# Kernel optimization log

Measured on AMD Instinct MI355X. Metric: run time of the kernel, lower is better.

The kernel has to match this reference:

```python
import jax, jax.numpy as jnp
import numpy as np

NUM_CLASSES = 4
SIGMA_S = 1.0
SIGMA_Z = 1.0


def _rbf_gram(x, sigma):
    # x: [N, d] -> [N, N] Gaussian kernel exp(-||xi-xj||^2 / (2 sigma^2))
    sq = jnp.sum(x * x, axis=-1)
    d2 = sq[:, None] + sq[None, :] - 2.0 * (x @ x.T)
    d2 = jnp.maximum(d2, 0.0)
    return jnp.exp(-d2 / (2.0 * sigma * sigma))


def _double_center(K):
    # Faithful to: K = mean_center(K, dim=0); K_m = mean_center(K.t(), dim=0)
    K = K - jnp.mean(K, axis=0, keepdims=True)
    K = K.T
    K = K - jnp.mean(K, axis=0, keepdims=True)
    return K


def setup_inputs() -> dict:
    key = jax.random.key(0)
    kz, ks = jax.random.split(key)
    z = jax.random.normal(kz, (8192, 128), dtype=jnp.float32)
    s = jax.random.randint(ks, (8192,), 0, NUM_CLASSES, dtype=jnp.int64)
    norm = jnp.float32(1.0)
    return {"z": z, "s": s, "norm": norm}


def reference(z, s, norm):
    n = z.shape[0]
    s_onehot = jax.nn.one_hot(s, NUM_CLASSES, dtype=z.dtype)  # format_onehot
    K_sm = _double_center(_rbf_gram(s_onehot, SIGMA_S))
    K_zm = _double_center(_rbf_gram(z, SIGMA_Z))
    # trace(K_zm.T @ K_sm) == sum(K_zm * K_sm): O(N^2) instead of O(N^3)
    dep = jnp.sum(K_zm * K_sm)
    dep = dep / (norm * (n * n))
    return dep
```

## Files before the change

kernel.cpp:

```cpp
#include <hip/hip_runtime.h>
#include <hip/hip_bf16.h>

typedef float f32x4 __attribute__((ext_vector_type(4)));

#define ZD      128
#define BT      128
#define D2_CUT  60.0f
#define D2_TRIG 70.0f

__device__ __forceinline__ void async_copy16(const unsigned char* g,
                                             unsigned char* l) {
    __builtin_amdgcn_global_load_lds(
        (const __attribute__((address_space(1))) unsigned int*)g,
        (__attribute__((address_space(3))) unsigned int*)l,
        16, 0, 0);
}

__global__ __launch_bounds__(256) void dep_prep(
    const float* __restrict__ z, const int* __restrict__ s,
    float* __restrict__ sq, float* __restrict__ sqmin,
    unsigned char* __restrict__ zb8, float* __restrict__ pvals,
    const float* __restrict__ norm, float* __restrict__ out, int N)
{
    __shared__ float part[32][33];
    const int tid  = threadIdx.x;
    const int wave = tid >> 6, lane = tid & 63;
    const int half = lane >> 5, c = lane & 31;
    const int r0   = blockIdx.x * 32;

    if (blockIdx.x == 0 && wave == 2) {
        int c0 = 0, c1 = 0, c2 = 0, c3 = 0;
        for (int it = lane; it < N / 4; it += 64) {
            int4 v = ((const int4*)s)[it];
            c0 += (v.x == 0) + (v.y == 0) + (v.z == 0) + (v.w == 0);
            c1 += (v.x == 1) + (v.y == 1) + (v.z == 1) + (v.w == 1);
            c2 += (v.x == 2) + (v.y == 2) + (v.z == 2) + (v.w == 2);
            c3 += (v.x == 3) + (v.y == 3) + (v.z == 3) + (v.w == 3);
        }
        #pragma unroll
        for (int off = 1; off < 64; off <<= 1) {
            c0 += __shfl_xor(c0, off, 64);
            c1 += __shfl_xor(c1, off, 64);
            c2 += __shfl_xor(c2, off, 64);
            c3 += __shfl_xor(c3, off, 64);
        }
        if (lane == 0) {
            const double n = (double)N;
            const double p0 = c0 / n, p1 = c1 / n, p2 = c2 / n, p3 = c3 / n;
            const double sump2 = p0*p0 + p1*p1 + p2*p2 + p3*p3;
            const double scale = (1.0 - exp(-1.0)) / ((double)norm[0] * n * n);
            pvals[0] = (float)p0; pvals[1] = (float)p1;
            pvals[2] = (float)p2; pvals[3] = (float)p3;
            pvals[4] = (float)sump2;
            pvals[5] = (float)scale;
            const double c2sum = (double)c0*c0 + (double)c1*c1
                               + (double)c2*c2 + (double)c3*c3;
            const double diag = n - c2sum / n;
            out[0] = (float)(diag * scale);
        }
    }

    #pragma unroll
    for (int i = 0; i < 4; ++i) {
        const int rloc = wave * 8 + i * 2 + half;
        const int r    = r0 + rloc;
        float4 v = ((const float4*)z)[r * 32 + c];
        int pk = __builtin_amdgcn_cvt_pk_fp8_f32(v.x, v.y, 0, false);
        pk     = __builtin_amdgcn_cvt_pk_fp8_f32(v.z, v.w, pk, true);
        ((unsigned int*)zb8)[r * 32 + c] = (unsigned int)pk;
        part[rloc][c] = v.x*v.x + v.y*v.y + v.z*v.z + v.w*v.w;
    }
    __syncthreads();

    if (wave == 0 && lane < 32) {
        float sum = 0.f;
        #pragma unroll
        for (int k = 0; k < 32; ++k) sum += part[lane][k];
        sq[r0 + lane] = sum;
        float mn = sum;
        #pragma unroll
        for (int off = 1; off < 32; off <<= 1)
            mn = fminf(mn, __shfl_xor(mn, off, 64));
        if (lane == 0) sqmin[blockIdx.x] = mn;
    }
}

__global__ __launch_bounds__(256, 4) void dep_pair(
    const unsigned char* __restrict__ zb8, const float* __restrict__ sq,
    const float* __restrict__ sqmin, const int* __restrict__ s,
    const float* __restrict__ pvals, float* __restrict__ out, int T)
{
    __shared__ unsigned char Apan[BT * ZD];
    __shared__ unsigned char Bpan[BT * ZD];

    const int tid  = threadIdx.x;
    const int wave = tid >> 6, lane = tid & 63;

    const int t = blockIdx.x;
    #define TRI_BASE(x) ((x) * T - ((x) * ((x) - 1)) / 2)
    double disc = (2.0 * T + 1.0) * (2.0 * T + 1.0) - 8.0 * (double)t;
    int ti = (int)((2.0 * T + 1.0 - sqrt(disc)) * 0.5);
    if (ti < 0) ti = 0;
    if (ti > T - 1) ti = T - 1;
    while (ti + 1 < T && TRI_BASE(ti + 1) <= t) ++ti;
    while (ti > 0 && TRI_BASE(ti) > t) --ti;
    const int tj = ti + (t - TRI_BASE(ti));
    #undef TRI_BASE

    const int i0 = ti * BT, j0 = tj * BT;
    const int wi = wave >> 1, wj = wave & 1;
    const int l15 = lane & 15, quad = lane >> 4;

    {
        const unsigned char* gAp = zb8 + (size_t)i0 * ZD;
        const unsigned char* gBp = zb8 + (size_t)j0 * ZD;
        const int rl  = lane >> 3;
        const int cch = lane & 7;
        const int gch = cch ^ rl;
        #pragma unroll
        for (int k = 0; k < 4; ++k) {
            const int r0i = (wave * 4 + k) * 8;
            const size_t go = (size_t)(r0i + rl) * ZD + (gch << 4);
            async_copy16(gAp + go, Apan + r0i * ZD);
            async_copy16(gBp + go, Bpan + r0i * ZD);
        }
    }
    __syncthreads();

    f32x4 accv[4][4];
    #pragma unroll
    for (int a = 0; a < 4; ++a)
        #pragma unroll
        for (int b = 0; b < 4; ++b)
            accv[a][b] = (f32x4){0.f, 0.f, 0.f, 0.f};

    const int sub = (quad & 1) * 8;
    #pragma unroll
    for (int kc = 0; kc < 4; ++kc) {
        long af[4], bfr[4];
        const int ch = (kc * 2 + (quad >> 1)) ^ (l15 & 7);
        #pragma unroll
        for (int it = 0; it < 4; ++it) {
            const int row = wi * 64 + it * 16 + l15;
            af[it] = *(const long*)(Apan + row * ZD + (ch << 4) + sub);
        }
        #pragma unroll
        for (int jt = 0; jt < 4; ++jt) {
            const int row = wj * 64 + jt * 16 + l15;
            bfr[jt] = *(const long*)(Bpan + row * ZD + (ch << 4) + sub);
        }
        #pragma unroll
        for (int it = 0; it < 4; ++it)
            #pragma unroll
            for (int jt = 0; jt < 4; ++jt)
                accv[it][jt] = __builtin_amdgcn_mfma_f32_16x16x32_fp8_fp8(
                    af[it], bfr[jt], accv[it][jt], 0, 0, 0);
    }

    float m = -1e30f;
    #pragma unroll
    for (int it = 0; it < 4; ++it)
        #pragma unroll
        for (int jt = 0; jt < 4; ++jt) {
            const f32x4 v = accv[it][jt];
            m = fmaxf(m, fmaxf(fmaxf(v[0], v[1]), fmaxf(v[2], v[3])));
        }
    #pragma unroll
    for (int off = 1; off < 64; off <<= 1)
        m = fmaxf(m, __shfl_xor(m, off, 64));

    const int gA = (i0 >> 5) + wi * 2;
    const int gB = (j0 >> 5) + wj * 2;
    const float sminA = fminf(sqmin[gA], sqmin[gA + 1]);
    const float sminB = fminf(sqmin[gB], sqmin[gB + 1]);
    const float bound = sminA + sminB - 2.0f * m;

    if (bound < D2_TRIG) {
        const float p0 = pvals[0], p1 = pvals[1],
                    p2 = pvals[2], p3 = pvals[3];
        const float sump2 = pvals[4], scale = pvals[5];
        const float p[4] = {p0, p1, p2, p3};

        const int ibase = i0 + wi * 64, jbase = j0 + wj * 64;
        float sqj[4];
        #pragma unroll
        for (int jt = 0; jt < 4; ++jt) sqj[jt] = sq[jbase + jt * 16 + l15];

        float local = 0.f;
        #pragma unroll
        for (int it = 0; it < 4; ++it) {
            #pragma unroll
            for (int r = 0; r < 4; ++r) {
                const int i = ibase + it * 16 + quad * 4 + r;
                const float sqi = sq[i];
                #pragma unroll
                for (int jt = 0; jt < 4; ++jt) {
                    const int j = jbase + jt * 16 + l15;
                    float d2 = sqi + sqj[jt] - 2.0f * accv[it][jt][r];
                    d2 = fmaxf(d2, 0.0f);
                    if (d2 < D2_CUT && i != j) {
                        const int si = s[i], sj = s[j];
                        const float w = (si == sj ? 1.0f : 0.0f)
                                      - p[si] - p[sj] + sump2;
                        local += w * __expf(-0.5f * d2);
                    }
                }
            }
        }
        if (ti < tj) local *= 2.0f;

        #pragma unroll
        for (int off = 32; off > 0; off >>= 1)
            local += __shfl_down(local, off, 64);
        if (lane == 0 && local != 0.0f)
            atomicAdd(out, local * scale);
    }
}

extern "C" void kernel_launch(void* const* d_in, const int* in_sizes, int n_in,
                              void* d_out, int out_size, void* d_ws, size_t ws_size,
                              hipStream_t stream)
{
    const float* z    = (const float*)d_in[0];
    const int*   s    = (const int*)d_in[1];
    const float* norm = (const float*)d_in[2];
    float* out = (float*)d_out;

    const int N = in_sizes[1];
    const int T = N / BT;

    char* ws = (char*)d_ws;
    float*         pvals = (float*)ws;
    float*         sq    = (float*)(ws + 64);
    float*         sqmin = (float*)(ws + 64 + (size_t)N * 4);
    unsigned char* zb8   = (unsigned char*)(ws + 64 + (size_t)N * 4
                                            + (size_t)(N / 32) * 4);

    dep_prep<<<N / 32, 256, 0, stream>>>(z, s, sq, sqmin, zb8, pvals,
                                         norm, out, N);
    const int nblocks = T * (T + 1) / 2;
    dep_pair<<<nblocks, 256, 0, stream>>>(zb8, sq, sqmin, s, pvals, out, T);
}
```

Baseline: 76.76 us.

## Fuse fp8 conversion and class counting into the pair kernel

```diff
diff --git a/kernel.cpp b/kernel.cpp
--- a/kernel.cpp
+++ b/kernel.cpp
@@ -1,5 +1,4 @@
 #include <hip/hip_runtime.h>
-#include <hip/hip_bf16.h>
 
 typedef float f32x4 __attribute__((ext_vector_type(4)));
 
@@ -8,90 +7,15 @@
 #define D2_CUT  60.0f
 #define D2_TRIG 70.0f
 
-__device__ __forceinline__ void async_copy16(const unsigned char* g,
-                                             unsigned char* l) {
-    __builtin_amdgcn_global_load_lds(
-        (const __attribute__((address_space(1))) unsigned int*)g,
-        (__attribute__((address_space(3))) unsigned int*)l,
-        16, 0, 0);
-}
-
-__global__ __launch_bounds__(256) void dep_prep(
+__global__ __launch_bounds__(256, 4) void dep_fused(
     const float* __restrict__ z, const int* __restrict__ s,
-    float* __restrict__ sq, float* __restrict__ sqmin,
-    unsigned char* __restrict__ zb8, float* __restrict__ pvals,
-    const float* __restrict__ norm, float* __restrict__ out, int N)
+    const float* __restrict__ norm, float* __restrict__ out,
+    int T, int N)
 {
-    __shared__ float part[32][33];
-    const int tid  = threadIdx.x;
-    const int wave = tid >> 6, lane = tid & 63;
-    const int half = lane >> 5, c = lane & 31;
-    const int r0   = blockIdx.x * 32;
-
-    if (blockIdx.x == 0 && wave == 2) {
-        int c0 = 0, c1 = 0, c2 = 0, c3 = 0;
-        for (int it = lane; it < N / 4; it += 64) {
-            int4 v = ((const int4*)s)[it];
-            c0 += (v.x == 0) + (v.y == 0) + (v.z == 0) + (v.w == 0);
-            c1 += (v.x == 1) + (v.y == 1) + (v.z == 1) + (v.w == 1);
-            c2 += (v.x == 2) + (v.y == 2) + (v.z == 2) + (v.w == 2);
-            c3 += (v.x == 3) + (v.y == 3) + (v.z == 3) + (v.w == 3);
-        }
-        #pragma unroll
-        for (int off = 1; off < 64; off <<= 1) {
-            c0 += __shfl_xor(c0, off, 64);
-            c1 += __shfl_xor(c1, off, 64);
-            c2 += __shfl_xor(c2, off, 64);
-            c3 += __shfl_xor(c3, off, 64);
-        }
-        if (lane == 0) {
-            const double n = (double)N;
-            const double p0 = c0 / n, p1 = c1 / n, p2 = c2 / n, p3 = c3 / n;
-            const double sump2 = p0*p0 + p1*p1 + p2*p2 + p3*p3;
-            const double scale = (1.0 - exp(-1.0)) / ((double)norm[0] * n * n);
-            pvals[0] = (float)p0; pvals[1] = (float)p1;
-            pvals[2] = (float)p2; pvals[3] = (float)p3;
-            pvals[4] = (float)sump2;
-            pvals[5] = (float)scale;
-            const double c2sum = (double)c0*c0 + (double)c1*c1
-                               + (double)c2*c2 + (double)c3*c3;
-            const double diag = n - c2sum / n;
-            out[0] = (float)(diag * scale);
-        }
-    }
-
-    #pragma unroll
-    for (int i = 0; i < 4; ++i) {
-        const int rloc = wave * 8 + i * 2 + half;
-        const int r    = r0 + rloc;
-        float4 v = ((const float4*)z)[r * 32 + c];
-        int pk = __builtin_amdgcn_cvt_pk_fp8_f32(v.x, v.y, 0, false);
-        pk     = __builtin_amdgcn_cvt_pk_fp8_f32(v.z, v.w, pk, true);
-        ((unsigned int*)zb8)[r * 32 + c] = (unsigned int)pk;
-        part[rloc][c] = v.x*v.x + v.y*v.y + v.z*v.z + v.w*v.w;
-    }
-    __syncthreads();
-
-    if (wave == 0 && lane < 32) {
-        float sum = 0.f;
-        #pragma unroll
-        for (int k = 0; k < 32; ++k) sum += part[lane][k];
-        sq[r0 + lane] = sum;
-        float mn = sum;
-        #pragma unroll
-        for (int off = 1; off < 32; off <<= 1)
-            mn = fminf(mn, __shfl_xor(mn, off, 64));
-        if (lane == 0) sqmin[blockIdx.x] = mn;
-    }
-}
-
-__global__ __launch_bounds__(256, 4) void dep_pair(
-    const unsigned char* __restrict__ zb8, const float* __restrict__ sq,
-    const float* __restrict__ sqmin, const int* __restrict__ s,
-    const float* __restrict__ pvals, float* __restrict__ out, int T)
-{
-    __shared__ unsigned char Apan[BT * ZD];
-    __shared__ unsigned char Bpan[BT * ZD];
+    __shared__ __align__(16) unsigned char Apan[BT * ZD];
+    __shared__ __align__(16) unsigned char Bpan[BT * ZD];
+    __shared__ float sqA[BT];
+    __shared__ float sqB[BT];
 
     const int tid  = threadIdx.x;
     const int wave = tid >> 6, lane = tid & 63;
@@ -112,18 +36,27 @@
     const int l15 = lane & 15, quad = lane >> 4;
 
     {
-        const unsigned char* gAp = zb8 + (size_t)i0 * ZD;
-        const unsigned char* gBp = zb8 + (size_t)j0 * ZD;
-        const int rl  = lane >> 3;
-        const int cch = lane & 7;
-        const int gch = cch ^ rl;
+        const int pr  = tid & 127;
+        const int isB = tid >> 7;
+        const int grow = (isB ? j0 : i0) + pr;
+        unsigned char* pan = isB ? Bpan : Apan;
+        const float4* zrow = (const float4*)(z + (size_t)grow * ZD);
+        float ssum = 0.f;
         #pragma unroll
-        for (int k = 0; k < 4; ++k) {
-            const int r0i = (wave * 4 + k) * 8;
-            const size_t go = (size_t)(r0i + rl) * ZD + (gch << 4);
-            async_copy16(gAp + go, Apan + r0i * ZD);
-            async_copy16(gBp + go, Bpan + r0i * ZD);
+        for (int gc = 0; gc < 8; ++gc) {
+            unsigned int w[4];
+            #pragma unroll
+            for (int q = 0; q < 4; ++q) {
+                const float4 v = zrow[gc * 4 + q];
+                ssum += v.x*v.x + v.y*v.y + v.z*v.z + v.w*v.w;
+                int pk = __builtin_amdgcn_cvt_pk_fp8_f32(v.x, v.y, 0, false);
+                pk     = __builtin_amdgcn_cvt_pk_fp8_f32(v.z, v.w, pk, true);
+                w[q] = (unsigned int)pk;
+            }
+            const int dch = gc ^ (pr & 7);
+            ((uint4*)(pan + pr * ZD))[dch] = make_uint4(w[0], w[1], w[2], w[3]);
         }
+        (isB ? sqB : sqA)[pr] = ssum;
     }
     __syncthreads();
 
@@ -165,37 +98,56 @@
             const f32x4 v = accv[it][jt];
             m = fmaxf(m, fmaxf(fmaxf(v[0], v[1]), fmaxf(v[2], v[3])));
         }
+    float sminA = sqA[wi * 64 + lane];
+    float sminB = sqB[wj * 64 + lane];
     #pragma unroll
-    for (int off = 1; off < 64; off <<= 1)
-        m = fmaxf(m, __shfl_xor(m, off, 64));
-
-    const int gA = (i0 >> 5) + wi * 2;
-    const int gB = (j0 >> 5) + wj * 2;
-    const float sminA = fminf(sqmin[gA], sqmin[gA + 1]);
-    const float sminB = fminf(sqmin[gB], sqmin[gB + 1]);
+    for (int off = 1; off < 64; off <<= 1) {
+        m     = fmaxf(m,     __shfl_xor(m, off, 64));
+        sminA = fminf(sminA, __shfl_xor(sminA, off, 64));
+        sminB = fminf(sminB, __shfl_xor(sminB, off, 64));
+    }
     const float bound = sminA + sminB - 2.0f * m;
 
     if (bound < D2_TRIG) {
-        const float p0 = pvals[0], p1 = pvals[1],
-                    p2 = pvals[2], p3 = pvals[3];
-        const float sump2 = pvals[4], scale = pvals[5];
-        const float p[4] = {p0, p1, p2, p3};
+        int c0 = 0, c1 = 0, c2 = 0, c3 = 0;
+        for (int it = lane; it < N / 4; it += 64) {
+            const int4 v = ((const int4*)s)[it];
+            c0 += (v.x == 0) + (v.y == 0) + (v.z == 0) + (v.w == 0);
+            c1 += (v.x == 1) + (v.y == 1) + (v.z == 1) + (v.w == 1);
+            c2 += (v.x == 2) + (v.y == 2) + (v.z == 2) + (v.w == 2);
+            c3 += (v.x == 3) + (v.y == 3) + (v.z == 3) + (v.w == 3);
+        }
+        #pragma unroll
+        for (int off = 1; off < 64; off <<= 1) {
+            c0 += __shfl_xor(c0, off, 64);
+            c1 += __shfl_xor(c1, off, 64);
+            c2 += __shfl_xor(c2, off, 64);
+            c3 += __shfl_xor(c3, off, 64);
+        }
+        const double nD = (double)N;
+        const double p0 = c0 / nD, p1 = c1 / nD, p2 = c2 / nD, p3 = c3 / nD;
+        const double sump2d = p0*p0 + p1*p1 + p2*p2 + p3*p3;
+        const double scaled = (1.0 - exp(-1.0)) / ((double)norm[0] * nD * nD);
+        const float p[4]   = {(float)p0, (float)p1, (float)p2, (float)p3};
+        const float sump2  = (float)sump2d;
+        const float scale  = (float)scaled;
 
-        const int ibase = i0 + wi * 64, jbase = j0 + wj * 64;
+        const int ibase = wi * 64, jbase = wj * 64;
         float sqj[4];
         #pragma unroll
-        for (int jt = 0; jt < 4; ++jt) sqj[jt] = sq[jbase + jt * 16 + l15];
+        for (int jt = 0; jt < 4; ++jt) sqj[jt] = sqB[jbase + jt * 16 + l15];
 
         float local = 0.f;
         #pragma unroll
         for (int it = 0; it < 4; ++it) {
             #pragma unroll
             for (int r = 0; r < 4; ++r) {
-                const int i = ibase + it * 16 + quad * 4 + r;
-                const float sqi = sq[i];
+                const int rloc = ibase + it * 16 + quad * 4 + r;
+                const int i    = i0 + rloc;
+                const float sqi = sqA[rloc];
                 #pragma unroll
                 for (int jt = 0; jt < 4; ++jt) {
-                    const int j = jbase + jt * 16 + l15;
+                    const int j = j0 + jbase + jt * 16 + l15;
                     float d2 = sqi + sqj[jt] - 2.0f * accv[it][jt][r];
                     d2 = fmaxf(d2, 0.0f);
                     if (d2 < D2_CUT && i != j) {
@@ -212,8 +164,16 @@
         #pragma unroll
         for (int off = 32; off > 0; off >>= 1)
             local += __shfl_down(local, off, 64);
-        if (lane == 0 && local != 0.0f)
-            atomicAdd(out, local * scale);
+
+        if (lane == 0) {
+            if (local != 0.0f) atomicAdd(out, local * scale);
+            if (t == 0 && wave == 0) {
+                const double c2sum = (double)c0*c0 + (double)c1*c1
+                                   + (double)c2*c2 + (double)c3*c3;
+                const double diag = nD - c2sum / nD;
+                atomicAdd(out, (float)(diag * scaled));
+            }
+        }
     }
 }
 
@@ -229,15 +189,10 @@
     const int N = in_sizes[1];
     const int T = N / BT;
 
-    char* ws = (char*)d_ws;
-    float*         pvals = (float*)ws;
-    float*         sq    = (float*)(ws + 64);
-    float*         sqmin = (float*)(ws + 64 + (size_t)N * 4);
-    unsigned char* zb8   = (unsigned char*)(ws + 64 + (size_t)N * 4
-                                            + (size_t)(N / 32) * 4);
+    (void)d_ws; (void)ws_size; (void)n_in; (void)out_size;
 
-    dep_prep<<<N / 32, 256, 0, stream>>>(z, s, sq, sqmin, zb8, pvals,
-                                         norm, out, N);
+    hipMemsetAsync(out, 0, sizeof(float), stream);
+
     const int nblocks = T * (T + 1) / 2;
-    dep_pair<<<nblocks, 256, 0, stream>>>(zb8, sq, sqmin, s, pvals, out, T);
+    dep_fused<<<nblocks, 256, 0, stream>>>(z, s, norm, out, T, N);
 }
```

Result: slower. 100.5 us (+31.0%).

## Process 2x2 super-tiles per block to reuse loaded panels across subtiles

Applied to the files above, without the earlier changes.

```diff
diff --git a/kernel.cpp b/kernel.cpp
--- a/kernel.cpp
+++ b/kernel.cpp
@@ -1,10 +1,10 @@
 #include <hip/hip_runtime.h>
-#include <hip/hip_bf16.h>
 
 typedef float f32x4 __attribute__((ext_vector_type(4)));
 
 #define ZD      128
 #define BT      128
+#define PAN     (BT * ZD)
 #define D2_CUT  60.0f
 #define D2_TRIG 70.0f
 
@@ -85,35 +85,34 @@
     }
 }
 
-__global__ __launch_bounds__(256, 4) void dep_pair(
+__global__ __launch_bounds__(256, 2) void dep_pair(
     const unsigned char* __restrict__ zb8, const float* __restrict__ sq,
     const float* __restrict__ sqmin, const int* __restrict__ s,
     const float* __restrict__ pvals, float* __restrict__ out, int T)
 {
-    __shared__ unsigned char Apan[BT * ZD];
-    __shared__ unsigned char Bpan[BT * ZD];
+    __shared__ unsigned char Apan[2 * PAN];
+    __shared__ unsigned char Bpan[2 * PAN];
 
     const int tid  = threadIdx.x;
     const int wave = tid >> 6, lane = tid & 63;
 
+    const int ST = T >> 1;
     const int t = blockIdx.x;
-    #define TRI_BASE(x) ((x) * T - ((x) * ((x) - 1)) / 2)
-    double disc = (2.0 * T + 1.0) * (2.0 * T + 1.0) - 8.0 * (double)t;
-    int ti = (int)((2.0 * T + 1.0 - sqrt(disc)) * 0.5);
-    if (ti < 0) ti = 0;
-    if (ti > T - 1) ti = T - 1;
-    while (ti + 1 < T && TRI_BASE(ti + 1) <= t) ++ti;
-    while (ti > 0 && TRI_BASE(ti) > t) --ti;
-    const int tj = ti + (t - TRI_BASE(ti));
+    #define TRI_BASE(x) ((x) * ST - ((x) * ((x) - 1)) / 2)
+    double disc = (2.0 * ST + 1.0) * (2.0 * ST + 1.0) - 8.0 * (double)t;
+    int I = (int)((2.0 * ST + 1.0 - sqrt(disc)) * 0.5);
+    if (I < 0) I = 0;
+    if (I > ST - 1) I = ST - 1;
+    while (I + 1 < ST && TRI_BASE(I + 1) <= t) ++I;
+    while (I > 0 && TRI_BASE(I) > t) --I;
+    const int J = I + (t - TRI_BASE(I));
     #undef TRI_BASE
 
-    const int i0 = ti * BT, j0 = tj * BT;
+    const int i0 = I * 2 * BT, j0 = J * 2 * BT;
     const int wi = wave >> 1, wj = wave & 1;
     const int l15 = lane & 15, quad = lane >> 4;
 
     {
-        const unsigned char* gAp = zb8 + (size_t)i0 * ZD;
-        const unsigned char* gBp = zb8 + (size_t)j0 * ZD;
         const int rl  = lane >> 3;
         const int cch = lane & 7;
         const int gch = cch ^ rl;
@@ -121,99 +120,117 @@
         for (int k = 0; k < 4; ++k) {
             const int r0i = (wave * 4 + k) * 8;
             const size_t go = (size_t)(r0i + rl) * ZD + (gch << 4);
-            async_copy16(gAp + go, Apan + r0i * ZD);
-            async_copy16(gBp + go, Bpan + r0i * ZD);
+            #pragma unroll
+            for (int p = 0; p < 2; ++p) {
+                async_copy16(zb8 + (size_t)(i0 + p * BT) * ZD + go,
+                             Apan + p * PAN + r0i * ZD);
+                async_copy16(zb8 + (size_t)(j0 + p * BT) * ZD + go,
+                             Bpan + p * PAN + r0i * ZD);
+            }
         }
     }
     __syncthreads();
 
-    f32x4 accv[4][4];
-    #pragma unroll
-    for (int a = 0; a < 4; ++a)
-        #pragma unroll
-        for (int b = 0; b < 4; ++b)
-            accv[a][b] = (f32x4){0.f, 0.f, 0.f, 0.f};
-
     const int sub = (quad & 1) * 8;
-    #pragma unroll
-    for (int kc = 0; kc < 4; ++kc) {
-        long af[4], bfr[4];
-        const int ch = (kc * 2 + (quad >> 1)) ^ (l15 & 7);
-        #pragma unroll
-        for (int it = 0; it < 4; ++it) {
-            const int row = wi * 64 + it * 16 + l15;
-            af[it] = *(const long*)(Apan + row * ZD + (ch << 4) + sub);
-        }
-        #pragma unroll
-        for (int jt = 0; jt < 4; ++jt) {
-            const int row = wj * 64 + jt * 16 + l15;
-            bfr[jt] = *(const long*)(Bpan + row * ZD + (ch << 4) + sub);
-        }
+
+    #pragma unroll 1
+    for (int st = 0; st < 4; ++st) {
+        const int a = st >> 1, b = st & 1;
+        const int tis = 2 * I + a, tjs = 2 * J + b;
+        if (tis > tjs) continue;
+
+        const unsigned char* Ap = Apan + a * PAN;
+        const unsigned char* Bp = Bpan + b * PAN;
+        const int i0s = i0 + a * BT, j0s = j0 + b * BT;
+
+        f32x4 accv[4][4];
+        #pragma unroll
+        for (int x = 0; x < 4; ++x)
+            #pragma unroll
+            for (int y = 0; y < 4; ++y)
+                accv[x][y] = (f32x4){0.f, 0.f, 0.f, 0.f};
+
+        #pragma unroll
+        for (int kc = 0; kc < 4; ++kc) {
+            long af[4], bfr[4];
+            const int ch = (kc * 2 + (quad >> 1)) ^ (l15 & 7);
+            #pragma unroll
+            for (int it = 0; it < 4; ++it) {
+                const int row = wi * 64 + it * 16 + l15;
+                af[it] = *(const long*)(Ap + row * ZD + (ch << 4) + sub);
+            }
+            #pragma unroll
+            for (int jt = 0; jt < 4; ++jt) {
+                const int row = wj * 64 + jt * 16 + l15;
+                bfr[jt] = *(const long*)(Bp + row * ZD + (ch << 4) + sub);
+            }
+            #pragma unroll
+            for (int it = 0; it < 4; ++it)
+                #pragma unroll
+                for (int jt = 0; jt < 4; ++jt)
+                    accv[it][jt] = __builtin_amdgcn_mfma_f32_16x16x32_fp8_fp8(
+                        af[it], bfr[jt], accv[it][jt], 0, 0, 0);
+        }
+
+        float m = -1e30f;
         #pragma unroll
         for (int it = 0; it < 4; ++it)
             #pragma unroll
+            for (int jt = 0; jt < 4; ++jt) {
+                const f32x4 v = accv[it][jt];
+                m = fmaxf(m, fmaxf(fmaxf(v[0], v[1]), fmaxf(v[2], v[3])));
+            }
+        #pragma unroll
+        for (int off = 1; off < 64; off <<= 1)
+            m = fmaxf(m, __shfl_xor(m, off, 64));
+
+        const int gA = (i0s >> 5) + wi * 2;
+        const int gB = (j0s >> 5) + wj * 2;
+        const float sminA = fminf(sqmin[gA], sqmin[gA + 1]);
+        const float sminB = fminf(sqmin[gB], sqmin[gB + 1]);
+        const float bound = sminA + sminB - 2.0f * m;
+
+        if (bound < D2_TRIG) {
+            const float p0 = pvals[0], p1 = pvals[1],
+                        p2 = pvals[2], p3 = pvals[3];
+            const float sump2 = pvals[4], scale = pvals[5];
+            const float p[4] = {p0, p1, p2, p3};
+
+            const int ibase = i0s + wi * 64, jbase = j0s + wj * 64;
+            float sqj[4];
+            #pragma unroll
             for (int jt = 0; jt < 4; ++jt)
-                accv[it][jt] = __builtin_amdgcn_mfma_f32_16x16x32_fp8_fp8(
-                    af[it], bfr[jt], accv[it][jt], 0, 0, 0);
-    }
-
-    float m = -1e30f;
-    #pragma unroll
-    for (int it = 0; it < 4; ++it)
-        #pragma unroll
-        for (int jt = 0; jt < 4; ++jt) {
-            const f32x4 v = accv[it][jt];
-            m = fmaxf(m, fmaxf(fmaxf(v[0], v[1]), fmaxf(v[2], v[3])));
-        }
-    #pragma unroll
-    for (int off = 1; off < 64; off <<= 1)
-        m = fmaxf(m, __shfl_xor(m, off, 64));
-
-    const int gA = (i0 >> 5) + wi * 2;
-    const int gB = (j0 >> 5) + wj * 2;
-    const float sminA = fminf(sqmin[gA], sqmin[gA + 1]);
-    const float sminB = fminf(sqmin[gB], sqmin[gB + 1]);
-    const float bound = sminA + sminB - 2.0f * m;
-
-    if (bound < D2_TRIG) {
-        const float p0 = pvals[0], p1 = pvals[1],
-                    p2 = pvals[2], p3 = pvals[3];
-        const float sump2 = pvals[4], scale = pvals[5];
-        const float p[4] = {p0, p1, p2, p3};
-
-        const int ibase = i0 + wi * 64, jbase = j0 + wj * 64;
-        float sqj[4];
-        #pragma unroll
-        for (int jt = 0; jt < 4; ++jt) sqj[jt] = sq[jbase + jt * 16 + l15];
-
-        float local = 0.f;
-        #pragma unroll
-        for (int it = 0; it < 4; ++it) {
-            #pragma unroll
-            for (int r = 0; r < 4; ++r) {
-                const int i = ibase + it * 16 + quad * 4 + r;
-                const float sqi = sq[i];
+                sqj[jt] = sq[jbase + jt * 16 + l15];
+
+            float local = 0.f;
+            #pragma unroll
+            for (int it = 0; it < 4; ++it) {
                 #pragma unroll
-                for (int jt = 0; jt < 4; ++jt) {
-                    const int j = jbase + jt * 16 + l15;
-                    float d2 = sqi + sqj[jt] - 2.0f * accv[it][jt][r];
-                    d2 = fmaxf(d2, 0.0f);
-                    if (d2 < D2_CUT && i != j) {
-                        const int si = s[i], sj = s[j];
-                        const float w = (si == sj ? 1.0f : 0.0f)
-                                      - p[si] - p[sj] + sump2;
-                        local += w * __expf(-0.5f * d2);
+                for (int r = 0; r < 4; ++r) {
+                    const int i = ibase + it * 16 + quad * 4 + r;
+                    const float sqi = sq[i];
+                    #pragma unroll
+                    for (int jt = 0; jt < 4; ++jt) {
+                        const int j = jbase + jt * 16 + l15;
+                        float d2 = sqi + sqj[jt] - 2.0f * accv[it][jt][r];
+                        d2 = fmaxf(d2, 0.0f);
+                        if (d2 < D2_CUT && i != j) {
+                            const int si = s[i], sj = s[j];
+                            const float w = (si == sj ? 1.0f : 0.0f)
+                                          - p[si] - p[sj] + sump2;
+                            local += w * __expf(-0.5f * d2);
+                        }
                     }
                 }
             }
-        }
-        if (ti < tj) local *= 2.0f;
-
-        #pragma unroll
-        for (int off = 32; off > 0; off >>= 1)
-            local += __shfl_down(local, off, 64);
-        if (lane == 0 && local != 0.0f)
-            atomicAdd(out, local * scale);
+            if (tis < tjs) local *= 2.0f;
+
+            #pragma unroll
+            for (int off = 32; off > 0; off >>= 1)
+                local += __shfl_down(local, off, 64);
+            if (lane == 0 && local != 0.0f)
+                atomicAdd(out, local * scale);
+        }
     }
 }
 
@@ -238,6 +255,7 @@
 
     dep_prep<<<N / 32, 256, 0, stream>>>(z, s, sq, sqmin, zb8, pvals,
                                          norm, out, N);
-    const int nblocks = T * (T + 1) / 2;
+    const int ST = T / 2;
+    const int nblocks = ST * (ST + 1) / 2;
     dep_pair<<<nblocks, 256, 0, stream>>>(zb8, sq, sqmin, s, pvals, out, T);
 }
```

After: 82.21 us. 7.1% more time.

## Use 128x64 rectangular tiles with element-level upper-triangle masking

Applied to the files above, without the earlier changes.

```diff
diff --git a/kernel.cpp b/kernel.cpp
--- a/kernel.cpp
+++ b/kernel.cpp
@@ -1,10 +1,10 @@
 #include <hip/hip_runtime.h>
-#include <hip/hip_bf16.h>
 
 typedef float f32x4 __attribute__((ext_vector_type(4)));
 
 #define ZD      128
-#define BT      128
+#define BTI     128
+#define BTJ     64
 #define D2_CUT  60.0f
 #define D2_TRIG 70.0f
 
@@ -18,15 +18,15 @@
 
 __global__ __launch_bounds__(256) void dep_prep(
     const float* __restrict__ z, const int* __restrict__ s,
-    float* __restrict__ sq, float* __restrict__ sqmin,
+    float* __restrict__ sq, float* __restrict__ sqmin8,
     unsigned char* __restrict__ zb8, float* __restrict__ pvals,
     const float* __restrict__ norm, float* __restrict__ out, int N)
 {
-    __shared__ float part[32][33];
+    __shared__ float part[8][33];
     const int tid  = threadIdx.x;
     const int wave = tid >> 6, lane = tid & 63;
     const int half = lane >> 5, c = lane & 31;
-    const int r0   = blockIdx.x * 32;
+    const int r0   = blockIdx.x * 8;
 
     if (blockIdx.x == 0 && wave == 2) {
         int c0 = 0, c1 = 0, c2 = 0, c3 = 0;
@@ -60,9 +60,8 @@
         }
     }
 
-    #pragma unroll
-    for (int i = 0; i < 4; ++i) {
-        const int rloc = wave * 8 + i * 2 + half;
+    {
+        const int rloc = wave * 2 + half;
         const int r    = r0 + rloc;
         float4 v = ((const float4*)z)[r * 32 + c];
         int pk = __builtin_amdgcn_cvt_pk_fp8_f32(v.x, v.y, 0, false);
@@ -72,72 +71,78 @@
     }
     __syncthreads();
 
-    if (wave == 0 && lane < 32) {
+    if (wave == 0 && lane < 8) {
         float sum = 0.f;
         #pragma unroll
         for (int k = 0; k < 32; ++k) sum += part[lane][k];
         sq[r0 + lane] = sum;
         float mn = sum;
         #pragma unroll
-        for (int off = 1; off < 32; off <<= 1)
+        for (int off = 1; off < 8; off <<= 1)
             mn = fminf(mn, __shfl_xor(mn, off, 64));
-        if (lane == 0) sqmin[blockIdx.x] = mn;
-    }
-}
-
-__global__ __launch_bounds__(256, 4) void dep_pair(
+        if (lane == 0) sqmin8[blockIdx.x] = mn;
+    }
+}
+
+__global__ __launch_bounds__(256, 6) void dep_pair(
     const unsigned char* __restrict__ zb8, const float* __restrict__ sq,
-    const float* __restrict__ sqmin, const int* __restrict__ s,
-    const float* __restrict__ pvals, float* __restrict__ out, int T)
+    const float* __restrict__ sqmin8, const int* __restrict__ s,
+    const float* __restrict__ pvals, float* __restrict__ out, int TJ)
 {
-    __shared__ unsigned char Apan[BT * ZD];
-    __shared__ unsigned char Bpan[BT * ZD];
+    __shared__ unsigned char Apan[BTI * ZD];
+    __shared__ unsigned char Bpan[BTJ * ZD];
 
     const int tid  = threadIdx.x;
     const int wave = tid >> 6, lane = tid & 63;
 
     const int t = blockIdx.x;
-    #define TRI_BASE(x) ((x) * T - ((x) * ((x) - 1)) / 2)
-    double disc = (2.0 * T + 1.0) * (2.0 * T + 1.0) - 8.0 * (double)t;
-    int ti = (int)((2.0 * T + 1.0 - sqrt(disc)) * 0.5);
+    #define TRI_BASE(x) ((x) * (TJ + 1 - (x)))
+    const int TI = TJ >> 1;
+    const float sf = sqrtf((float)((TJ + 1) * (TJ + 1) - 4 * t));
+    int ti = (int)(((float)(TJ + 1) - sf) * 0.5f);
     if (ti < 0) ti = 0;
-    if (ti > T - 1) ti = T - 1;
-    while (ti + 1 < T && TRI_BASE(ti + 1) <= t) ++ti;
+    if (ti > TI - 1) ti = TI - 1;
+    while (ti + 1 < TI && TRI_BASE(ti + 1) <= t) ++ti;
     while (ti > 0 && TRI_BASE(ti) > t) --ti;
-    const int tj = ti + (t - TRI_BASE(ti));
+    const int tj2 = 2 * ti + (t - TRI_BASE(ti));
     #undef TRI_BASE
 
-    const int i0 = ti * BT, j0 = tj * BT;
-    const int wi = wave >> 1, wj = wave & 1;
+    const int i0 = ti * BTI, j0 = tj2 * BTJ;
+    const int wi = wave >> 1;
+    const int wj = wave & 1;
     const int l15 = lane & 15, quad = lane >> 4;
 
     {
-        const unsigned char* gAp = zb8 + (size_t)i0 * ZD;
-        const unsigned char* gBp = zb8 + (size_t)j0 * ZD;
         const int rl  = lane >> 3;
         const int cch = lane & 7;
         const int gch = cch ^ rl;
+        const size_t goff = (size_t)rl * ZD + (gch << 4);
+        const unsigned char* gAp = zb8 + (size_t)i0 * ZD;
+        const unsigned char* gBp = zb8 + (size_t)j0 * ZD;
         #pragma unroll
         for (int k = 0; k < 4; ++k) {
             const int r0i = (wave * 4 + k) * 8;
-            const size_t go = (size_t)(r0i + rl) * ZD + (gch << 4);
-            async_copy16(gAp + go, Apan + r0i * ZD);
-            async_copy16(gBp + go, Bpan + r0i * ZD);
+            async_copy16(gAp + (size_t)r0i * ZD + goff, Apan + r0i * ZD);
+        }
+        #pragma unroll
+        for (int k = 0; k < 2; ++k) {
+            const int r0i = (wave * 2 + k) * 8;
+            async_copy16(gBp + (size_t)r0i * ZD + goff, Bpan + r0i * ZD);
         }
     }
     __syncthreads();
 
-    f32x4 accv[4][4];
+    f32x4 accv[4][2];
     #pragma unroll
     for (int a = 0; a < 4; ++a)
         #pragma unroll
-        for (int b = 0; b < 4; ++b)
+        for (int b = 0; b < 2; ++b)
             accv[a][b] = (f32x4){0.f, 0.f, 0.f, 0.f};
 
     const int sub = (quad & 1) * 8;
     #pragma unroll
     for (int kc = 0; kc < 4; ++kc) {
-        long af[4], bfr[4];
+        long af[4], bfr[2];
         const int ch = (kc * 2 + (quad >> 1)) ^ (l15 & 7);
         #pragma unroll
         for (int it = 0; it < 4; ++it) {
@@ -145,14 +150,14 @@
             af[it] = *(const long*)(Apan + row * ZD + (ch << 4) + sub);
         }
         #pragma unroll
-        for (int jt = 0; jt < 4; ++jt) {
-            const int row = wj * 64 + jt * 16 + l15;
+        for (int jt = 0; jt < 2; ++jt) {
+            const int row = wj * 32 + jt * 16 + l15;
             bfr[jt] = *(const long*)(Bpan + row * ZD + (ch << 4) + sub);
         }
         #pragma unroll
         for (int it = 0; it < 4; ++it)
             #pragma unroll
-            for (int jt = 0; jt < 4; ++jt)
+            for (int jt = 0; jt < 2; ++jt)
                 accv[it][jt] = __builtin_amdgcn_mfma_f32_16x16x32_fp8_fp8(
                     af[it], bfr[jt], accv[it][jt], 0, 0, 0);
     }
@@ -161,7 +166,7 @@
     #pragma unroll
     for (int it = 0; it < 4; ++it)
         #pragma unroll
-        for (int jt = 0; jt < 4; ++jt) {
+        for (int jt = 0; jt < 2; ++jt) {
             const f32x4 v = accv[it][jt];
             m = fmaxf(m, fmaxf(fmaxf(v[0], v[1]), fmaxf(v[2], v[3])));
         }
@@ -169,10 +174,15 @@
     for (int off = 1; off < 64; off <<= 1)
         m = fmaxf(m, __shfl_xor(m, off, 64));
 
-    const int gA = (i0 >> 5) + wi * 2;
-    const int gB = (j0 >> 5) + wj * 2;
-    const float sminA = fminf(sqmin[gA], sqmin[gA + 1]);
-    const float sminB = fminf(sqmin[gB], sqmin[gB + 1]);
+    const int ibase = i0 + wi * 64, jbase = j0 + wj * 32;
+    const int gA = ibase >> 3;
+    const int gB = jbase >> 3;
+    float sminA = sqmin8[gA];
+    #pragma unroll
+    for (int k = 1; k < 8; ++k) sminA = fminf(sminA, sqmin8[gA + k]);
+    float sminB = sqmin8[gB];
+    #pragma unroll
+    for (int k = 1; k < 4; ++k) sminB = fminf(sminB, sqmin8[gB + k]);
     const float bound = sminA + sminB - 2.0f * m;
 
     if (bound < D2_TRIG) {
@@ -181,10 +191,9 @@
         const float sump2 = pvals[4], scale = pvals[5];
         const float p[4] = {p0, p1, p2, p3};
 
-        const int ibase = i0 + wi * 64, jbase = j0 + wj * 64;
-        float sqj[4];
-        #pragma unroll
-        for (int jt = 0; jt < 4; ++jt) sqj[jt] = sq[jbase + jt * 16 + l15];
+        float sqj[2];
+        #pragma unroll
+        for (int jt = 0; jt < 2; ++jt) sqj[jt] = sq[jbase + jt * 16 + l15];
 
         float local = 0.f;
         #pragma unroll
@@ -194,11 +203,11 @@
                 const int i = ibase + it * 16 + quad * 4 + r;
                 const float sqi = sq[i];
                 #pragma unroll
-                for (int jt = 0; jt < 4; ++jt) {
+                for (int jt = 0; jt < 2; ++jt) {
                     const int j = jbase + jt * 16 + l15;
                     float d2 = sqi + sqj[jt] - 2.0f * accv[it][jt][r];
                     d2 = fmaxf(d2, 0.0f);
-                    if (d2 < D2_CUT && i != j) {
+                    if (d2 < D2_CUT && j > i) {
                         const int si = s[i], sj = s[j];
                         const float w = (si == sj ? 1.0f : 0.0f)
                                       - p[si] - p[sj] + sump2;
@@ -207,7 +216,7 @@
                 }
             }
         }
-        if (ti < tj) local *= 2.0f;
+        local *= 2.0f;
 
         #pragma unroll
         for (int off = 32; off > 0; off >>= 1)
@@ -226,18 +235,19 @@
     const float* norm = (const float*)d_in[2];
     float* out = (float*)d_out;
 
-    const int N = in_sizes[1];
-    const int T = N / BT;
+    const int N  = in_sizes[1];
+    const int TI = N / BTI;
+    const int TJ = N / BTJ;
 
     char* ws = (char*)d_ws;
-    float*         pvals = (float*)ws;
-    float*         sq    = (float*)(ws + 64);
-    float*         sqmin = (float*)(ws + 64 + (size_t)N * 4);
-    unsigned char* zb8   = (unsigned char*)(ws + 64 + (size_t)N * 4
-                                            + (size_t)(N / 32) * 4);
-
-    dep_prep<<<N / 32, 256, 0, stream>>>(z, s, sq, sqmin, zb8, pvals,
-                                         norm, out, N);
-    const int nblocks = T * (T + 1) / 2;
-    dep_pair<<<nblocks, 256, 0, stream>>>(zb8, sq, sqmin, s, pvals, out, T);
-}
+    float*         pvals  = (float*)ws;
+    float*         sq     = (float*)(ws + 64);
+    float*         sqmin8 = (float*)(ws + 64 + (size_t)N * 4);
+    unsigned char* zb8    = (unsigned char*)(ws + 64 + (size_t)N * 4
+                                             + (size_t)(N / 8) * 4);
+
+    dep_prep<<<N / 8, 256, 0, stream>>>(z, s, sq, sqmin8, zb8, pvals,
+                                        norm, out, N);
+    const int nblocks = TI * TJ - TI * (TI - 1);
+    dep_pair<<<nblocks, 256, 0, stream>>>(zb8, sq, sqmin8, s, pvals, out, TJ);
+}
```

Result: no change. 77.55 us (+1.0%).
